# Optimization experiments

Measured on AMD Instinct MI355X. Metric: run time of the kernel, lower is better.

Reference implementation:

```python
import jax, jax.numpy as jnp
import numpy as np

N, H, W, PD, HID, NH = 2, 64, 64, 16, 128, 4
EPS = 1e-5


def _bn(x, g, b):
    # training-mode BatchNorm over (N, H, W) with biased variance, channels last
    m = jnp.mean(x, axis=(0, 1, 2), keepdims=True)
    v = jnp.var(x, axis=(0, 1, 2), keepdims=True)
    return (x - m) * jax.lax.rsqrt(v + EPS) * g + b


def _mha(x, in_w, in_b, out_w, out_b, nh):
    # torch nn.MultiheadAttention (batch_first) with packed qkv in_proj
    B, S, E = x.shape
    hd = E // nh
    q, k, v = jnp.split(x @ in_w.T + in_b, 3, axis=-1)
    def heads(t):
        return t.reshape(B, S, nh, hd).transpose(0, 2, 1, 3)  # B,nh,S,hd
    q, k, v = heads(q), heads(k), heads(v)
    a = jax.nn.softmax(jnp.einsum('bnqd,bnkd->bnqk', q, k) / np.float32(np.sqrt(hd)), axis=-1)
    o = jnp.einsum('bnqk,bnkd->bnqd', a, v).transpose(0, 2, 1, 3).reshape(B, S, E)
    return o @ out_w.T + out_b


def setup_inputs():
    key = jax.random.key(0)
    ks = jax.random.split(key, 32)
    def r(i, shape, s=0.1):
        return jax.random.normal(ks[i], shape, dtype=jnp.float32) * s
    mask = (jnp.arange(W) % 2) == 0  # alternating columns kept, M = W//2
    return {
        'kspace': jax.random.normal(ks[0], (N, 2, H, W), dtype=jnp.float32),
        'mask': mask,
        'pre_conv_w': r(1, (PD, 2), 0.5), 'pre_conv_b': r(2, (PD,)),
        'pre_pe_H': r(3, (H, PD)), 'pre_pe_W': r(4, (W, PD)),
        'res_conv1_w': r(5, (PD, PD), 0.2), 'res_conv1_b': r(6, (PD,)),
        'res_bn1_g': 1.0 + r(7, (PD,)), 'res_bn1_b': r(8, (PD,)),
        'res_conv2_w': r(9, (PD, PD), 0.2), 'res_conv2_b': r(10, (PD,)),
        'res_bn2_g': 1.0 + r(11, (PD,)), 'res_bn2_b': r(12, (PD,)),
        'proj_w': r(13, (HID, PD), 0.2), 'proj_b': r(14, (HID,)),
        'enc_in_w': r(15, (3 * HID, HID), 0.08), 'enc_in_b': r(16, (3 * HID,)),
        'enc_out_w': r(17, (HID, HID), 0.08), 'enc_out_b': r(18, (HID,)),
        'dec_pe_H': r(19, (H, HID)), 'dec_pe_W': r(20, (W, HID)),
        'dec_in_w': r(21, (3 * HID, HID), 0.08), 'dec_in_b': r(22, (3 * HID,)),
        'dec_out_w': r(23, (HID, HID), 0.08), 'dec_out_b': r(24, (HID,)),
        'masked_token': r(25, (HID,), 1.0),
        'post_w': r(26, (2, HID), 0.1), 'post_b': r(27, (2,)),
    }


def reference(kspace, mask, pre_conv_w, pre_conv_b, pre_pe_H, pre_pe_W,
              res_conv1_w, res_conv1_b, res_bn1_g, res_bn1_b,
              res_conv2_w, res_conv2_b, res_bn2_g, res_bn2_b,
              proj_w, proj_b, enc_in_w, enc_in_b, enc_out_w, enc_out_b,
              dec_pe_H, dec_pe_W, dec_in_w, dec_in_b, dec_out_w, dec_out_b,
              masked_token, post_w, post_b):
    cols = np.nonzero(np.asarray(mask))[0]  # static sampled columns
    M = cols.shape[0]
    # gather valid columns; channels last: [N, H, M, 2]
    x = kspace.transpose(0, 2, 3, 1)[:, :, cols, :]
    h = x @ pre_conv_w.T + pre_conv_b  # 1x1 conv -> [N, H, M, PD]
    h = h + (pre_pe_H[:, None, :] + pre_pe_W[cols][None, :, :])
    # PixelwiseConstantChannelResNet (1 layer)
    r1 = jax.nn.relu(_bn(h @ res_conv1_w.T + res_conv1_b, res_bn1_g, res_bn1_b))
    r2 = jax.nn.relu(_bn(r1 @ res_conv2_w.T + res_conv2_b, res_bn2_g, res_bn2_b))
    h = jax.nn.relu(h + r2)
    h = h @ proj_w.T + proj_b  # [N, H, M, HID]
    enc = _mha(h.reshape(N, H * M, HID), enc_in_w, enc_in_b, enc_out_w, enc_out_b, NH)
    # scatter: fill unmasked positions with masked_token, masked with encoder output
    dec = jnp.broadcast_to(masked_token, (N, H, W, HID))
    dec = dec.at[:, :, cols, :].set(enc.reshape(N, H, M, HID))
    dec = dec + (dec_pe_H[:, None, :] + dec_pe_W[None, :, :])
    dec = _mha(dec.reshape(N, H * W, HID), dec_in_w, dec_in_b, dec_out_w, dec_out_b, NH)
    out = dec.reshape(N, H, W, HID) @ post_w.T + post_b  # [N, H, W, 2]
    return out.transpose(0, 3, 1, 2)  # [N, 2, H, W]
```

## Files before the change

### kernel.cpp

```cpp
#include <hip/hip_runtime.h>
#include <math.h>

#define N_ 2
#define H_ 64
#define W_ 64
#define M_ 32
#define PD_ 16
#define HID_ 128
#define NH_ 4
#define HD_ 32
#define S_ENC 2048
#define S_DEC 4096
#define EPS_ 1e-5f
#define SCALE_ 0.17677669529663687f
#define SCALE2_ (0.17677669529663687f * 1.4426950408889634f)

#define OFF_H     0
#define OFF_T1    65536
#define OFF_T2    131072
#define OFF_STAT  196608
#define OFF_WP    196672
#define OFF_BP    202816
#define OFF_QBF   203264
#define OFF_KBF   727552
#define OFF_VTBF  1251840
#define OFF_ATTBF 1776128
#define OFF_XBF2  2300416
#define OFF_WBF   2824704

#define WOFF_ENC_OUT 0
#define WOFF_DEC_IN  16384
#define WOFF_DEC_OUT 65536

#define IB_MF   2048
#define IB_WC   320
#define IB_WP   24
#define IB_BP   2
#define IB_TOT  (IB_MF + IB_WC + IB_WP + IB_BP + 1)

typedef short bf16x8 __attribute__((ext_vector_type(8)));
typedef short bf16x4 __attribute__((ext_vector_type(4)));
typedef float f32x4 __attribute__((ext_vector_type(4)));

__device__ __forceinline__ short f2bf(float f) {
  union { float f; unsigned u; } v; v.f = f;
  unsigned r = v.u + 0x7FFFu + ((v.u >> 16) & 1u);
  return (short)(r >> 16);
}

__global__ void k_init(const float* __restrict__ eow, const float* __restrict__ dw,
                       const float* __restrict__ dow, const float* __restrict__ mt,
                       const float* __restrict__ peH, const float* __restrict__ peW,
                       const float* __restrict__ ew, const float* __restrict__ pw,
                       const float* __restrict__ pb, const float* __restrict__ eib,
                       short* __restrict__ wbf, short* __restrict__ xdec,
                       float* __restrict__ wp, float* __restrict__ bp,
                       float* __restrict__ stat) {
  int blk = blockIdx.x, tid = threadIdx.x;
  if (blk < IB_MF) {
    int idx = blk * 256 + tid;
    int j = idx & 127;
    int widx = (idx >> 7) & 31;
    int hh = (idx >> 12) & 63;
    int b = idx >> 18;
    int w = 2 * widx + 1;
    xdec[((size_t)(b * 4096 + hh * 64 + w)) * 128 + j] =
        f2bf(mt[j] + peH[hh * 128 + j] + peW[w * 128 + j]);
  } else if (blk < IB_MF + IB_WC) {
    int idx = (blk - IB_MF) * 256 + tid;
    float v;
    if (idx < 16384) v = eow[idx];
    else if (idx < 65536) v = dw[idx - 16384];
    else v = dow[idx - 65536];
    wbf[idx] = f2bf(v);
  } else if (blk < IB_MF + IB_WC + IB_WP) {
    int e = (blk - IB_MF - IB_WC) * 256 + tid;
    int row = e >> 4, k = e & 15;
    float a = 0.f;
    for (int j = 0; j < 128; j++) a = fmaf(ew[row * 128 + j], pw[j * 16 + k], a);
    wp[e] = a;
  } else if (blk < IB_MF + IB_WC + IB_WP + IB_BP) {
    int row = (blk - IB_MF - IB_WC - IB_WP) * 256 + tid;
    if (row < 384) {
      float a = eib[row];
      for (int j = 0; j < 128; j++) a = fmaf(ew[row * 128 + j], pb[j], a);
      bp[row] = a;
    }
  } else {
    if (tid < 64) stat[tid] = 0.f;
  }
}

__global__ void k_prelin_stats(const float* __restrict__ ks, const float* __restrict__ pcw,
                               const float* __restrict__ pcb, const float* __restrict__ peH,
                               const float* __restrict__ peW, const float* __restrict__ w1,
                               const float* __restrict__ b1, float* __restrict__ h,
                               float* __restrict__ t1, float* __restrict__ stat) {
  int tid = threadIdx.x;
  int pos = blockIdx.x * 256 + tid;
  int m = pos & 31, hh = (pos >> 5) & 63, b = pos >> 11;
  int w = 2 * m;
  float x0 = ks[((b * 2 + 0) * H_ + hh) * W_ + w];
  float x1 = ks[((b * 2 + 1) * H_ + hh) * W_ + w];
  float hv[16], tv[16];
#pragma unroll
  for (int c = 0; c < 16; c++)
    hv[c] = x0 * pcw[c * 2] + x1 * pcw[c * 2 + 1] + pcb[c]
            + peH[hh * PD_ + c] + peW[w * PD_ + c];
#pragma unroll
  for (int c = 0; c < 16; c += 4)
    *(float4*)&h[pos * 16 + c] = make_float4(hv[c], hv[c + 1], hv[c + 2], hv[c + 3]);
#pragma unroll
  for (int c = 0; c < 16; c++) {
    float a = b1[c];
#pragma unroll
    for (int k = 0; k < 16; k++) a = fmaf(hv[k], w1[c * 16 + k], a);
    tv[c] = a;
    t1[pos * 16 + c] = a;
  }
  __shared__ float tl[256][17];
#pragma unroll
  for (int c = 0; c < 16; c++) tl[tid][c] = tv[c];
  __syncthreads();
  int c = tid & 15, g = tid >> 4;
  float s = 0.f, s2 = 0.f;
#pragma unroll
  for (int r = 0; r < 16; r++) {
    float v = tl[g * 16 + r][c];
    s += v; s2 += v * v;
  }
  __shared__ float ps[16][16], ps2[16][16];
  ps[g][c] = s; ps2[g][c] = s2;
  __syncthreads();
  if (tid < 16) {
    float S = 0.f, S2 = 0.f;
#pragma unroll
    for (int g2 = 0; g2 < 16; g2++) { S += ps[g2][tid]; S2 += ps2[g2][tid]; }
    atomicAdd(&stat[tid], S);
    atomicAdd(&stat[16 + tid], S2);
  }
}

__global__ void k_bnlin_stats(const float* __restrict__ t1, const float* __restrict__ stat,
                              const float* __restrict__ g1, const float* __restrict__ bb1,
                              const float* __restrict__ w2, const float* __restrict__ b2,
                              float* __restrict__ t2, float* __restrict__ statw) {
  int tid = threadIdx.x;
  int pos = blockIdx.x * 256 + tid;
  const float inv = 1.f / 4096.f;
  float r[16];
#pragma unroll
  for (int k = 0; k < 16; k++) {
    float mu = stat[k] * inv;
    float var = stat[16 + k] * inv - mu * mu;
    float v = (t1[pos * 16 + k] - mu) * rsqrtf(var + EPS_) * g1[k] + bb1[k];
    r[k] = fmaxf(v, 0.f);
  }
  float tv[16];
#pragma unroll
  for (int c = 0; c < 16; c++) {
    float a = b2[c];
#pragma unroll
    for (int k = 0; k < 16; k++) a = fmaf(r[k], w2[c * 16 + k], a);
    tv[c] = a;
    t2[pos * 16 + c] = a;
  }
  __shared__ float tl[256][17];
#pragma unroll
  for (int c = 0; c < 16; c++) tl[tid][c] = tv[c];
  __syncthreads();
  int c = tid & 15, g = tid >> 4;
  float s = 0.f, s2 = 0.f;
#pragma unroll
  for (int rr = 0; rr < 16; rr++) {
    float v = tl[g * 16 + rr][c];
    s += v; s2 += v * v;
  }
  __shared__ float ps[16][16], ps2[16][16];
  ps[g][c] = s; ps2[g][c] = s2;
  __syncthreads();
  if (tid < 16) {
    float S = 0.f, S2 = 0.f;
#pragma unroll
    for (int g2 = 0; g2 < 16; g2++) { S += ps[g2][tid]; S2 += ps2[g2][tid]; }
    atomicAdd(&statw[32 + tid], S);
    atomicAdd(&statw[48 + tid], S2);
  }
}

__global__ __launch_bounds__(256)
void k_fqkv_enc(const float* __restrict__ h, const float* __restrict__ t2,
                const float* __restrict__ stat, const float* __restrict__ g2,
                const float* __restrict__ bb2, const float* __restrict__ wp,
                const float* __restrict__ bp, short* __restrict__ qbf,
                short* __restrict__ kbf, short* __restrict__ vtbf) {
  int tid = threadIdx.x;
  int p0 = blockIdx.x * 32;
  __shared__ float hf[32][20];
  const float inv = 1.f / 4096.f;
#pragma unroll
  for (int i = 0; i < 2; i++) {
    int idx = tid * 2 + i;
    int lp = idx >> 4, c = idx & 15;
    int pos = p0 + lp;
    float mu = stat[32 + c] * inv;
    float var = stat[48 + c] * inv - mu * mu;
    float v = (t2[pos * 16 + c] - mu) * rsqrtf(var + EPS_) * g2[c] + bb2[c];
    v = fmaxf(v, 0.f);
    hf[lp][c] = fmaxf(h[pos * 16 + c] + v, 0.f);
  }
  __syncthreads();
  int bb = p0 >> 11;
  int sbase = p0 & 2047;
  {
    int col = tid;
    float wc[16];
#pragma unroll
    for (int k = 0; k < 16; k += 4) *(float4*)&wc[k] = *(const float4*)&wp[col * 16 + k];
    float bpv = bp[col];
    int isQ = (col < 128);
    int c2 = isQ ? col : (col - 128);
    int hd = c2 >> 5, d = c2 & 31;
    short* dst = isQ ? qbf : kbf;
    float sc = isQ ? SCALE2_ : 1.f;
    size_t rowb = ((size_t)(bb * 4 + hd) * S_ENC + sbase) * 32 + d;
    for (int lp = 0; lp < 32; lp++) {
      float a = bpv;
#pragma unroll
      for (int k = 0; k < 16; k++) a = fmaf(hf[lp][k], wc[k], a);
      dst[rowb + (size_t)lp * 32] = f2bf(a * sc);
    }
  }
  if (tid < 128) {
    int col = 256 + tid;
    float wc[16];
#pragma unroll
    for (int k = 0; k < 16; k += 4) *(float4*)&wc[k] = *(const float4*)&wp[col * 16 + k];
    float bpv = bp[col];
    int c2 = tid;
    int hd = c2 >> 5, d = c2 & 31;
    size_t rowb = ((size_t)(bb * 4 + hd) * 32 + d) * S_ENC + sbase;
    for (int lp4 = 0; lp4 < 32; lp4 += 4) {
      bf16x4 pk;
#pragma unroll
      for (int r = 0; r < 4; r++) {
        float a = bpv;
#pragma unroll
        for (int k = 0; k < 16; k++) a = fmaf(hf[lp4 + r][k], wc[k], a);
        pk[r] = f2bf(a);
      }
      *(bf16x4*)&vtbf[rowb + lp4] = pk;
    }
  }
}

#define MGEMM_STAGE_AND_FRAGS                                                   \
  __shared__ short As[64 * 128];                                                \
  __shared__ short Wl[64 * 128];                                                \
  int tid = threadIdx.x;                                                        \
  _Pragma("unroll")                                                             \
  for (int i = 0; i < 4; i++) {                                                 \
    int idx = i * 256 + tid;                                                    \
    int row = idx >> 4, c = idx & 15, slot = c ^ (row & 7);                     \
    *(bf16x8*)&As[row * 128 + slot * 8] =                                       \
        *(const bf16x8*)&abf[(size_t)(rb + row) * 128 + c * 8];                 \
    *(bf16x8*)&Wl[row * 128 + slot * 8] =                                       \
        *(const bf16x8*)&wbf[(size_t)(ob + row) * 128 + c * 8];                 \
  }                                                                             \
  __syncthreads();                                                              \
  int lane = tid & 63, wv = tid >> 6;                                           \
  int l15 = lane & 15, quad = lane >> 4;                                        \
  int m0 = wv * 16;                                                             \
  f32x4 acc[4];                                                                 \
  acc[0] = acc[1] = acc[2] = acc[3] = (f32x4){0.f, 0.f, 0.f, 0.f};              \
  _Pragma("unroll")                                                             \
  for (int kk = 0; kk < 4; kk++) {                                              \
    int sl = ((kk * 4 + quad) ^ (l15 & 7)) * 8;                                 \
    bf16x8 af = *(const bf16x8*)&As[(m0 + l15) * 128 + sl];                     \
    _Pragma("unroll")                                                           \
    for (int nt = 0; nt < 4; nt++) {                                            \
      bf16x8 wf = *(const bf16x8*)&Wl[(nt * 16 + l15) * 128 + sl];              \
      acc[nt] = __builtin_amdgcn_mfma_f32_16x16x32_bf16(af, wf, acc[nt], 0, 0, 0); \
    }                                                                           \
  }

__global__ __launch_bounds__(256)
void k_mgemm_qkv_dec(const short* __restrict__ abf, const short* __restrict__ wbf,
                     const float* __restrict__ bias, short* __restrict__ qbf,
                     short* __restrict__ kbf, short* __restrict__ vtbf) {
  const int S = 4096;
  int rb = blockIdx.x * 64, ob = blockIdx.y * 64;
  MGEMM_STAGE_AND_FRAGS
#pragma unroll
  for (int nt = 0; nt < 4; nt++) {
    int col = ob + nt * 16 + l15;
    float bv = bias[col];
    if (ob < 128) {
      int hd = col >> 5, d = col & 31;
#pragma unroll
      for (int r = 0; r < 4; r++) {
        int grow = rb + m0 + quad * 4 + r;
        int bb = grow >> 12, s = grow & (S - 1);
        qbf[((size_t)(bb * 4 + hd) * S + s) * 32 + d] =
            f2bf((acc[nt][r] + bv) * SCALE2_);
      }
    } else if (ob < 256) {
      int c2 = col - 128, hd = c2 >> 5, d = c2 & 31;
#pragma unroll
      for (int r = 0; r < 4; r++) {
        int grow = rb + m0 + quad * 4 + r;
        int bb = grow >> 12, s = grow & (S - 1);
        kbf[((size_t)(bb * 4 + hd) * S + s) * 32 + d] = f2bf(acc[nt][r] + bv);
      }
    } else {
      int c2 = col - 256, hd = c2 >> 5, d = c2 & 31;
      int grow0 = rb + m0 + quad * 4;
      int bb = grow0 >> 12, s0 = grow0 & (S - 1);
      bf16x4 pk;
#pragma unroll
      for (int r = 0; r < 4; r++) pk[r] = f2bf(acc[nt][r] + bv);
      *(bf16x4*)&vtbf[((size_t)(bb * 4 + hd) * 32 + d) * S + s0] = pk;
    }
  }
}

__global__ __launch_bounds__(256)
void k_mgemm_out_enc(const short* __restrict__ abf, const short* __restrict__ wbf,
                     const float* __restrict__ bias, const float* __restrict__ peH,
                     const float* __restrict__ peW, short* __restrict__ xdec) {
  int rb = blockIdx.x * 64, ob = blockIdx.y * 64;
  MGEMM_STAGE_AND_FRAGS
#pragma unroll
  for (int nt = 0; nt < 4; nt++) {
    int col = ob + nt * 16 + l15;
    float bv = bias[col];
#pragma unroll
    for (int r = 0; r < 4; r++) {
      int grow = rb + m0 + quad * 4 + r;
      int bb = grow >> 11, rem = grow & 2047;
      int hhh = rem >> 5, m = rem & 31, w = 2 * m;
      xdec[((size_t)(bb * 4096 + hhh * 64 + w)) * 128 + col] =
          f2bf(acc[nt][r] + bv + peH[hhh * 128 + col] + peW[w * 128 + col]);
    }
  }
}

__global__ __launch_bounds__(256)
void k_mgemm_out_post(const short* __restrict__ abf, const short* __restrict__ wbf,
                      const float* __restrict__ bias, const float* __restrict__ pw,
                      const float* __restrict__ pb, float* __restrict__ outp) {
  int rb = blockIdx.x * 64;
  __shared__ short As[64 * 128];
  __shared__ short Wl[128 * 128];
  int tid = threadIdx.x;
#pragma unroll
  for (int i = 0; i < 4; i++) {
    int idx = i * 256 + tid;
    int row = idx >> 4, c = idx & 15, slot = c ^ (row & 7);
    *(bf16x8*)&As[row * 128 + slot * 8] =
        *(const bf16x8*)&abf[(size_t)(rb + row) * 128 + c * 8];
  }
#pragma unroll
  for (int i = 0; i < 8; i++) {
    int idx = i * 256 + tid;
    int row = idx >> 4, c = idx & 15, slot = c ^ (row & 7);
    *(bf16x8*)&Wl[row * 128 + slot * 8] =
        *(const bf16x8*)&wbf[(size_t)row * 128 + c * 8];
  }
  __syncthreads();
  int lane = tid & 63, wv = tid >> 6;
  int l15 = lane & 15, quad = lane >> 4;
  int m0 = wv * 16;
  f32x4 acc[8];
#pragma unroll
  for (int nt = 0; nt < 8; nt++) acc[nt] = (f32x4){0.f, 0.f, 0.f, 0.f};
#pragma unroll
  for (int kk = 0; kk < 4; kk++) {
    int sl = ((kk * 4 + quad) ^ (l15 & 7)) * 8;
    bf16x8 af = *(const bf16x8*)&As[(m0 + l15) * 128 + sl];
#pragma unroll
    for (int nt = 0; nt < 8; nt++) {
      bf16x8 wf = *(const bf16x8*)&Wl[(nt * 16 + l15) * 128 + sl];
      acc[nt] = __builtin_amdgcn_mfma_f32_16x16x32_bf16(af, wf, acc[nt], 0, 0, 0);
    }
  }
  float bv[8], pw0[8], pw1[8];
#pragma unroll
  for (int nt = 0; nt < 8; nt++) {
    int col = nt * 16 + l15;
    bv[nt] = bias[col];
    pw0[nt] = pw[col];
    pw1[nt] = pw[128 + col];
  }
  float pb0 = pb[0], pb1 = pb[1];
#pragma unroll
  for (int r = 0; r < 4; r++) {
    float pc0 = 0.f, pc1 = 0.f;
#pragma unroll
    for (int nt = 0; nt < 8; nt++) {
      float yv = acc[nt][r] + bv[nt];
      pc0 = fmaf(yv, pw0[nt], pc0);
      pc1 = fmaf(yv, pw1[nt], pc1);
    }
    pc0 += __shfl_xor(pc0, 1); pc0 += __shfl_xor(pc0, 2);
    pc0 += __shfl_xor(pc0, 4); pc0 += __shfl_xor(pc0, 8);
    pc1 += __shfl_xor(pc1, 1); pc1 += __shfl_xor(pc1, 2);
    pc1 += __shfl_xor(pc1, 4); pc1 += __shfl_xor(pc1, 8);
    if (l15 == 0) {
      int grow = rb + m0 + quad * 4 + r;
      int bb = grow >> 12, hw = grow & 4095;
      outp[(size_t)(bb * 2 + 0) * 4096 + hw] = pc0 + pb0;
      outp[(size_t)(bb * 2 + 1) * 4096 + hw] = pc1 + pb1;
    }
  }
}

template <int S>
__global__ __launch_bounds__(1024)
__attribute__((amdgpu_waves_per_eu(8)))
void k_attn15(const short* __restrict__ qbf, const short* __restrict__ kbf,
              const short* __restrict__ vtbf, short* __restrict__ outb) {
  __shared__ __align__(16) char smem[65536];
  short* kb4 = (short*)smem;
  short* vt4 = (short*)(smem + 32768);
  float* abuf = (float*)smem;
  float* lb   = (float*)(smem + 24576);

  int qt = blockIdx.x, hh = blockIdx.y, b = blockIdx.z;
  int tid = threadIdx.x;
  int lane = tid & 63;
  int wv = tid >> 6;
  int qtr = wv >> 2;
  int wv4 = wv & 3;
  int l15 = lane & 15, quad = lane >> 4;
  int t256 = tid & 255;

  int bh = b * NH_ + hh;
  const short* kg = kbf + (size_t)bh * S * 32;
  const short* vg = vtbf + (size_t)bh * 32 * S;
  short* kbh = kb4 + qtr * 2048;
  short* vth = vt4 + qtr * 2048;

  bf16x8 qf = *(const bf16x8*)&qbf[((size_t)bh * S + qt * 64 + wv4 * 16 + l15) * 32
                                   + quad * 8];

  f32x4 acc[2];
  acc[0] = (f32x4){0.f, 0.f, 0.f, 0.f};
  acc[1] = (f32x4){0.f, 0.f, 0.f, 0.f};
  f32x4 accl = (f32x4){0.f, 0.f, 0.f, 0.f};
  const short ONEB = (short)0x3F80;
  const bf16x8 ones = {ONEB, ONEB, ONEB, ONEB, ONEB, ONEB, ONEB, ONEB};

  int srowK = t256 >> 2, schK = t256 & 3;
  int slotK = schK ^ ((srowK >> 1) & 3);
  int srowV = t256 >> 3, sslV = t256 & 7;
  int sgV = sslV ^ (srowV & 7);
  int gbV = ((sgV >> 2) << 5) + ((sgV & 3) << 2);

  int kq0 = qtr * (S / 4);
  int kxor = (l15 >> 1) & 3;
  int vsl = l15 & 7;

  const short* kgp = kg + (size_t)(kq0 + srowK) * 32 + schK * 8;
  const short* vgp0 = vg + (size_t)srowV * S + kq0 + gbV;
  const short* vgp1 = vgp0 + 16;
  short* kdst = kbh + srowK * 32 + slotK * 8;
  short* vdst = vth + srowV * 64 + sslV * 8;

  bf16x8 krg = *(const bf16x8*)kgp;
  bf16x4 vr0 = *(const bf16x4*)vgp0;
  bf16x4 vr1 = *(const bf16x4*)vgp1;

  constexpr int NIT = S / 256;
  for (int it = 0; it < NIT; ++it) {
    int co = (it & 1) << 13;
    *(bf16x8*)(kdst + co) = krg;
    *(bf16x8*)(vdst + co) = __builtin_shufflevector(vr0, vr1, 0, 1, 2, 3, 4, 5, 6, 7);
    if (it + 1 < NIT) {
      kgp += 64 * 32;
      vgp0 += 64;
      vgp1 += 64;
      krg = *(const bf16x8*)kgp;
      vr0 = *(const bf16x4*)vgp0;
      vr1 = *(const bf16x4*)vgp1;
    }
    asm volatile("s_waitcnt lgkmcnt(0)" ::: "memory");
    __builtin_amdgcn_s_barrier();
    asm volatile("" ::: "memory");

    const short* kbhc = kbh + co;
    const short* vthc = vth + co;

    f32x4 s[4];
#pragma unroll
    for (int t = 0; t < 4; t++) {
      bf16x8 kf = *(const bf16x8*)&kbhc[(t * 16 + l15) * 32 + ((quad ^ kxor) * 8)];
      s[t] = __builtin_amdgcn_mfma_f32_16x16x32_bf16(
          kf, qf, (f32x4){0.f, 0.f, 0.f, 0.f}, 0, 0, 0);
    }

    float pe[4][4];
#pragma unroll
    for (int t = 0; t < 4; t++) {
      pe[t][0] = __builtin_exp2f(s[t][0]);
      pe[t][1] = __builtin_exp2f(s[t][1]);
      pe[t][2] = __builtin_exp2f(s[t][2]);
      pe[t][3] = __builtin_exp2f(s[t][3]);
    }

#pragma unroll
    for (int kh = 0; kh < 2; kh++) {
      union { unsigned u[4]; bf16x8 v; } pf;
      asm("v_cvt_pk_bf16_f32 %0, %1, %2"
          : "=v"(pf.u[0]) : "v"(pe[2 * kh][0]), "v"(pe[2 * kh][1]));
      asm("v_cvt_pk_bf16_f32 %0, %1, %2"
          : "=v"(pf.u[1]) : "v"(pe[2 * kh][2]), "v"(pe[2 * kh][3]));
      asm("v_cvt_pk_bf16_f32 %0, %1, %2"
          : "=v"(pf.u[2]) : "v"(pe[2 * kh + 1][0]), "v"(pe[2 * kh + 1][1]));
      asm("v_cvt_pk_bf16_f32 %0, %1, %2"
          : "=v"(pf.u[3]) : "v"(pe[2 * kh + 1][2]), "v"(pe[2 * kh + 1][3]));
#pragma unroll
      for (int nt = 0; nt < 2; nt++) {
        bf16x8 vf = *(const bf16x8*)&vthc[(nt * 16 + l15) * 64
                                          + (((kh * 4 + quad) ^ vsl) * 8)];
        acc[nt] = __builtin_amdgcn_mfma_f32_16x16x32_bf16(vf, pf.v, acc[nt], 0, 0, 0);
      }
      accl = __builtin_amdgcn_mfma_f32_16x16x32_bf16(ones, pf.v, accl, 0, 0, 0);
    }
  }

  float lpart = accl[0];

  __syncthreads();
  if (qtr > 0) {
#pragma unroll
    for (int nt = 0; nt < 2; nt++)
#pragma unroll
      for (int r = 0; r < 4; r++)
        abuf[(qtr - 1) * 2048 + wv4 * 512 + (nt * 16 + quad * 4 + r) * 16 + l15] =
            acc[nt][r];
    if (quad == 0) lb[(qtr - 1) * 64 + wv4 * 16 + l15] = lpart;
  }
  __syncthreads();
  if (qtr == 0) {
    int li = wv4 * 16 + l15;
    float ltot = lpart + lb[li] + lb[64 + li] + lb[128 + li];
    float inv = 1.f / ltot;
    int base = wv4 * 512;
    short* op = outb + ((size_t)(b * S + qt * 64 + wv4 * 16 + l15)) * 128 + hh * 32;
#pragma unroll
    for (int nt = 0; nt < 2; nt++) {
      bf16x4 pk;
#pragma unroll
      for (int r = 0; r < 4; r++) {
        int d = nt * 16 + quad * 4 + r;
        float v = acc[nt][r] + abuf[base + d * 16 + l15]
                + abuf[2048 + base + d * 16 + l15]
                + abuf[4096 + base + d * 16 + l15];
        pk[r] = f2bf(v * inv);
      }
      *(bf16x4*)&op[nt * 16 + quad * 4] = pk;
    }
  }
}

template <int S>
__global__ __launch_bounds__(1024, 4)
void k_attn16(const short* __restrict__ qbf, const short* __restrict__ kbf,
              const short* __restrict__ vtbf, short* __restrict__ outb) {
  __shared__ __align__(16) char smem[65536];
  short* kb4 = (short*)smem;
  short* vt4 = (short*)(smem + 32768);
  float* abuf = (float*)smem;
  float* lb   = (float*)(smem + 49152);

  int qt = blockIdx.x, hh = blockIdx.y, b = blockIdx.z;
  int tid = threadIdx.x;
  int lane = tid & 63;
  int wv = tid >> 6;
  int qtr = wv >> 2;
  int qsub = wv & 3;
  int l15 = lane & 15, quad = lane >> 4;
  int t256 = tid & 255;

  int bh = b * NH_ + hh;
  const short* kg = kbf + (size_t)bh * S * 32;
  const short* vg = vtbf + (size_t)bh * 32 * S;
  short* kbh = kb4 + qtr * 2048;
  short* vth = vt4 + qtr * 2048;

  const short* qrow = &qbf[((size_t)bh * S + qt * 128 + qsub * 32 + l15) * 32
                           + quad * 8];
  bf16x8 qf0 = *(const bf16x8*)qrow;
  bf16x8 qf1 = *(const bf16x8*)(qrow + 16 * 32);

  f32x4 acc00 = {0.f,0.f,0.f,0.f}, acc01 = {0.f,0.f,0.f,0.f};
  f32x4 acc10 = {0.f,0.f,0.f,0.f}, acc11 = {0.f,0.f,0.f,0.f};
  f32x4 accl0 = {0.f,0.f,0.f,0.f}, accl1 = {0.f,0.f,0.f,0.f};
  const short ONEB = (short)0x3F80;
  const bf16x8 ones = {ONEB, ONEB, ONEB, ONEB, ONEB, ONEB, ONEB, ONEB};

  int srowK = t256 >> 2, schK = t256 & 3;
  int slotK = schK ^ ((srowK >> 1) & 3);
  int srowV = t256 >> 3, sslV = t256 & 7;
  int sgV = sslV ^ (srowV & 7);
  int gbV = ((sgV >> 2) << 5) + ((sgV & 3) << 2);

  int kq0 = qtr * (S / 4);
  int kxor = (l15 >> 1) & 3;
  int vsl = l15 & 7;

  const short* kgp = kg + (size_t)(kq0 + srowK) * 32 + schK * 8;
  const short* vgp0 = vg + (size_t)srowV * S + kq0 + gbV;
  const short* vgp1 = vgp0 + 16;
  short* kdst = kbh + srowK * 32 + slotK * 8;
  short* vdst = vth + srowV * 64 + sslV * 8;

  bf16x8 krg = *(const bf16x8*)kgp;
  bf16x4 vr0 = *(const bf16x4*)vgp0;
  bf16x4 vr1 = *(const bf16x4*)vgp1;

  constexpr int NIT = S / 256;
  for (int it = 0; it < NIT; ++it) {
    int co = (it & 1) << 13;
    *(bf16x8*)(kdst + co) = krg;
    *(bf16x8*)(vdst + co) = __builtin_shufflevector(vr0, vr1, 0, 1, 2, 3, 4, 5, 6, 7);
    if (it + 1 < NIT) {
      kgp += 64 * 32;
      vgp0 += 64;
      vgp1 += 64;
      krg = *(const bf16x8*)kgp;
      vr0 = *(const bf16x4*)vgp0;
      vr1 = *(const bf16x4*)vgp1;
    }
    asm volatile("s_waitcnt lgkmcnt(0)" ::: "memory");
    __builtin_amdgcn_s_barrier();
    asm volatile("" ::: "memory");

    const short* kbhc = kbh + co;
    const short* vthc = vth + co;

    f32x4 s0[4], s1[4];
#pragma unroll
    for (int t = 0; t < 4; t++) {
      bf16x8 kf = *(const bf16x8*)&kbhc[(t * 16 + l15) * 32 + ((quad ^ kxor) * 8)];
      s0[t] = __builtin_amdgcn_mfma_f32_16x16x32_bf16(
          kf, qf0, (f32x4){0.f, 0.f, 0.f, 0.f}, 0, 0, 0);
      s1[t] = __builtin_amdgcn_mfma_f32_16x16x32_bf16(
          kf, qf1, (f32x4){0.f, 0.f, 0.f, 0.f}, 0, 0, 0);
    }

#pragma unroll
    for (int kh = 0; kh < 2; kh++) {
      bf16x8 vfa = *(const bf16x8*)&vthc[(0 * 16 + l15) * 64
                                         + (((kh * 4 + quad) ^ vsl) * 8)];
      bf16x8 vfb = *(const bf16x8*)&vthc[(1 * 16 + l15) * 64
                                         + (((kh * 4 + quad) ^ vsl) * 8)];
      {
        float pa0 = __builtin_exp2f(s0[2 * kh][0]);
        float pa1 = __builtin_exp2f(s0[2 * kh][1]);
        float pa2 = __builtin_exp2f(s0[2 * kh][2]);
        float pa3 = __builtin_exp2f(s0[2 * kh][3]);
        float pb0v = __builtin_exp2f(s0[2 * kh + 1][0]);
        float pb1v = __builtin_exp2f(s0[2 * kh + 1][1]);
        float pb2v = __builtin_exp2f(s0[2 * kh + 1][2]);
        float pb3v = __builtin_exp2f(s0[2 * kh + 1][3]);
        union { unsigned u[4]; bf16x8 v; } pf;
        asm("v_cvt_pk_bf16_f32 %0, %1, %2" : "=v"(pf.u[0]) : "v"(pa0), "v"(pa1));
        asm("v_cvt_pk_bf16_f32 %0, %1, %2" : "=v"(pf.u[1]) : "v"(pa2), "v"(pa3));
        asm("v_cvt_pk_bf16_f32 %0, %1, %2" : "=v"(pf.u[2]) : "v"(pb0v), "v"(pb1v));
        asm("v_cvt_pk_bf16_f32 %0, %1, %2" : "=v"(pf.u[3]) : "v"(pb2v), "v"(pb3v));
        acc00 = __builtin_amdgcn_mfma_f32_16x16x32_bf16(vfa, pf.v, acc00, 0, 0, 0);
        acc01 = __builtin_amdgcn_mfma_f32_16x16x32_bf16(vfb, pf.v, acc01, 0, 0, 0);
        accl0 = __builtin_amdgcn_mfma_f32_16x16x32_bf16(ones, pf.v, accl0, 0, 0, 0);
      }
      {
        float pa0 = __builtin_exp2f(s1[2 * kh][0]);
        float pa1 = __builtin_exp2f(s1[2 * kh][1]);
        float pa2 = __builtin_exp2f(s1[2 * kh][2]);
        float pa3 = __builtin_exp2f(s1[2 * kh][3]);
        float pb0v = __builtin_exp2f(s1[2 * kh + 1][0]);
        float pb1v = __builtin_exp2f(s1[2 * kh + 1][1]);
        float pb2v = __builtin_exp2f(s1[2 * kh + 1][2]);
        float pb3v = __builtin_exp2f(s1[2 * kh + 1][3]);
        union { unsigned u[4]; bf16x8 v; } pf;
        asm("v_cvt_pk_bf16_f32 %0, %1, %2" : "=v"(pf.u[0]) : "v"(pa0), "v"(pa1));
        asm("v_cvt_pk_bf16_f32 %0, %1, %2" : "=v"(pf.u[1]) : "v"(pa2), "v"(pa3));
        asm("v_cvt_pk_bf16_f32 %0, %1, %2" : "=v"(pf.u[2]) : "v"(pb0v), "v"(pb1v));
        asm("v_cvt_pk_bf16_f32 %0, %1, %2" : "=v"(pf.u[3]) : "v"(pb2v), "v"(pb3v));
        acc10 = __builtin_amdgcn_mfma_f32_16x16x32_bf16(vfa, pf.v, acc10, 0, 0, 0);
        acc11 = __builtin_amdgcn_mfma_f32_16x16x32_bf16(vfb, pf.v, acc11, 0, 0, 0);
        accl1 = __builtin_amdgcn_mfma_f32_16x16x32_bf16(ones, pf.v, accl1, 0, 0, 0);
      }
    }
  }

  __syncthreads();
  if (qtr > 0) {
    float* ab = abuf + (qtr - 1) * 4096 + (qsub * 2) * 512;
#pragma unroll
    for (int r = 0; r < 4; r++) {
      ab[(0 * 16 + quad * 4 + r) * 16 + l15] = acc00[r];
      ab[(1 * 16 + quad * 4 + r) * 16 + l15] = acc01[r];
      ab[512 + (0 * 16 + quad * 4 + r) * 16 + l15] = acc10[r];
      ab[512 + (1 * 16 + quad * 4 + r) * 16 + l15] = acc11[r];
    }
    if (quad == 0) {
      lb[(qtr - 1) * 128 + qsub * 32 + l15] = accl0[0];
      lb[(qtr - 1) * 128 + qsub * 32 + 16 + l15] = accl1[0];
    }
  }
  __syncthreads();
  if (qtr == 0) {
#pragma unroll
    for (int j = 0; j < 2; j++) {
      int li = qsub * 32 + j * 16 + l15;
      float lpart = (j == 0) ? accl0[0] : accl1[0];
      float ltot = lpart + lb[li] + lb[128 + li] + lb[256 + li];
      float inv = 1.f / ltot;
      int base = (qsub * 2 + j) * 512;
      f32x4 a0 = (j == 0) ? acc00 : acc10;
      f32x4 a1 = (j == 0) ? acc01 : acc11;
      short* op = outb + ((size_t)(b * S + qt * 128 + li)) * 128 + hh * 32;
#pragma unroll
      for (int nt = 0; nt < 2; nt++) {
        bf16x4 pk;
#pragma unroll
        for (int r = 0; r < 4; r++) {
          int d = nt * 16 + quad * 4 + r;
          float v = ((nt == 0) ? a0[r] : a1[r])
                  + abuf[base + d * 16 + l15]
                  + abuf[4096 + base + d * 16 + l15]
                  + abuf[8192 + base + d * 16 + l15];
          pk[r] = f2bf(v * inv);
        }
        *(bf16x4*)&op[nt * 16 + quad * 4] = pk;
      }
    }
  }
}

extern "C" void kernel_launch(void* const* d_in, const int* in_sizes, int n_in,
                              void* d_out, int out_size, void* d_ws, size_t ws_size,
                              hipStream_t stream) {
  const float* ks        = (const float*)d_in[0];
  const float* pre_conv_w = (const float*)d_in[2];
  const float* pre_conv_b = (const float*)d_in[3];
  const float* pre_pe_H   = (const float*)d_in[4];
  const float* pre_pe_W   = (const float*)d_in[5];
  const float* w1  = (const float*)d_in[6];
  const float* b1  = (const float*)d_in[7];
  const float* g1  = (const float*)d_in[8];
  const float* bb1 = (const float*)d_in[9];
  const float* w2  = (const float*)d_in[10];
  const float* b2  = (const float*)d_in[11];
  const float* g2  = (const float*)d_in[12];
  const float* bb2 = (const float*)d_in[13];
  const float* proj_w = (const float*)d_in[14];
  const float* proj_b = (const float*)d_in[15];
  const float* enc_in_w  = (const float*)d_in[16];
  const float* enc_in_b  = (const float*)d_in[17];
  const float* enc_out_w = (const float*)d_in[18];
  const float* enc_out_b = (const float*)d_in[19];
  const float* dec_pe_H  = (const float*)d_in[20];
  const float* dec_pe_W  = (const float*)d_in[21];
  const float* dec_in_w  = (const float*)d_in[22];
  const float* dec_in_b  = (const float*)d_in[23];
  const float* dec_out_w = (const float*)d_in[24];
  const float* dec_out_b = (const float*)d_in[25];
  const float* masked_token = (const float*)d_in[26];
  const float* post_w = (const float*)d_in[27];
  const float* post_b = (const float*)d_in[28];
  float* out = (float*)d_out;

  float* ws    = (float*)d_ws;
  float* h     = ws + OFF_H;
  float* t1    = ws + OFF_T1;
  float* t2    = ws + OFF_T2;
  float* stat  = ws + OFF_STAT;
  float* wp    = ws + OFF_WP;
  float* bp    = ws + OFF_BP;
  short* qbf   = (short*)(ws + OFF_QBF);
  short* kbfb  = (short*)(ws + OFF_KBF);
  short* vtbfb = (short*)(ws + OFF_VTBF);
  short* attbf = (short*)(ws + OFF_ATTBF);
  short* xbf2  = (short*)(ws + OFF_XBF2);
  short* wbf   = (short*)(ws + OFF_WBF);

  k_init<<<IB_TOT, 256, 0, stream>>>(enc_out_w, dec_in_w, dec_out_w, masked_token,
                                     dec_pe_H, dec_pe_W, enc_in_w, proj_w, proj_b,
                                     enc_in_b, wbf, xbf2, wp, bp, stat);
  k_prelin_stats<<<16, 256, 0, stream>>>(ks, pre_conv_w, pre_conv_b, pre_pe_H,
                                         pre_pe_W, w1, b1, h, t1, stat);
  k_bnlin_stats<<<16, 256, 0, stream>>>(t1, stat, g1, bb1, w2, b2, t2, stat);
  k_fqkv_enc<<<128, 256, 0, stream>>>(h, t2, stat, g2, bb2, wp, bp,
                                      qbf, kbfb, vtbfb);
  k_attn15<S_ENC><<<dim3(S_ENC / 64, NH_, N_), 1024, 0, stream>>>(qbf, kbfb, vtbfb, attbf);
  k_mgemm_out_enc<<<dim3(S_ENC * N_ / 64, 2), 256, 0, stream>>>(
      attbf, wbf + WOFF_ENC_OUT, enc_out_b, dec_pe_H, dec_pe_W, xbf2);
  k_mgemm_qkv_dec<<<dim3(S_DEC * N_ / 64, 6), 256, 0, stream>>>(
      xbf2, wbf + WOFF_DEC_IN, dec_in_b, qbf, kbfb, vtbfb);
  k_attn16<S_DEC><<<dim3(S_DEC / 128, NH_, N_), 1024, 0, stream>>>(qbf, kbfb, vtbfb, attbf);
  k_mgemm_out_post<<<S_DEC * N_ / 64, 256, 0, stream>>>(
      attbf, wbf + WOFF_DEC_OUT, dec_out_b, post_w, post_b, out);
}
```

Baseline: 196.1 us.

## Split decoder attention keys across blocks and merge partials in out-projection

The decoder attention kernel no longer uses 1024-thread blocks that split the keys four ways and reduce through shared memory. It now launches 256-thread blocks that each handle half of the keys for one head. Each block writes its unnormalized bf16 partial output and float row-sum to workspace. The output-projection GEMM then adds the two halves and applies the normalization while loading its A tile. This removes the in-block LDS reduction and barriers and allows more, smaller blocks, at the cost of extra global traffic for the partials and an extra bf16 rounding step before the combine.

```diff
diff --git a/kernel.cpp b/kernel.cpp
--- a/kernel.cpp
+++ b/kernel.cpp
@@ -46,6 +46,12 @@
   union { float f; unsigned u; } v; v.f = f;
   unsigned r = v.u + 0x7FFFu + ((v.u >> 16) & 1u);
   return (short)(r >> 16);
+}
+
+__device__ __forceinline__ float bf2f(short s) {
+  union { unsigned u; float f; } v;
+  v.u = ((unsigned)(unsigned short)s) << 16;
+  return v.f;
 }
 
 __global__ void k_init(const float* __restrict__ eow, const float* __restrict__ dw,
@@ -346,9 +352,12 @@
 }
 
 __global__ __launch_bounds__(256)
-void k_mgemm_out_post(const short* __restrict__ abf, const short* __restrict__ wbf,
+void k_mgemm_out_post(const short* __restrict__ pbf, const float* __restrict__ lp,
+                      const short* __restrict__ wbf,
                       const float* __restrict__ bias, const float* __restrict__ pw,
                       const float* __restrict__ pb, float* __restrict__ outp) {
+  const int S = 4096;
+  const size_t HSTRIDE = (size_t)N_ * S * 128;
   int rb = blockIdx.x * 64;
   __shared__ short As[64 * 128];
   __shared__ short Wl[128 * 128];
@@ -357,8 +366,18 @@
   for (int i = 0; i < 4; i++) {
     int idx = i * 256 + tid;
     int row = idx >> 4, c = idx & 15, slot = c ^ (row & 7);
-    *(bf16x8*)&As[row * 128 + slot * 8] =
-        *(const bf16x8*)&abf[(size_t)(rb + row) * 128 + c * 8];
+    int grow = rb + row;
+    int bb = grow >> 12, q = grow & (S - 1);
+    int hh = c >> 2;
+    size_t lidx = (size_t)(bb * 4 + hh) * S + q;
+    float lt = lp[lidx] + lp[(size_t)8 * S + lidx];
+    float inv = 1.f / lt;
+    bf16x8 p0 = *(const bf16x8*)&pbf[(size_t)grow * 128 + c * 8];
+    bf16x8 p1 = *(const bf16x8*)&pbf[HSTRIDE + (size_t)grow * 128 + c * 8];
+    bf16x8 o;
+#pragma unroll
+    for (int j = 0; j < 8; j++) o[j] = f2bf((bf2f(p0[j]) + bf2f(p1[j])) * inv);
+    *(bf16x8*)&As[row * 128 + slot * 8] = o;
   }
 #pragma unroll
   for (int i = 0; i < 8; i++) {
@@ -565,29 +584,21 @@
 }
 
 template <int S>
-__global__ __launch_bounds__(1024, 4)
-void k_attn16(const short* __restrict__ qbf, const short* __restrict__ kbf,
-              const short* __restrict__ vtbf, short* __restrict__ outb) {
-  __shared__ __align__(16) char smem[65536];
-  short* kb4 = (short*)smem;
-  short* vt4 = (short*)(smem + 32768);
-  float* abuf = (float*)smem;
-  float* lb   = (float*)(smem + 49152);
-
-  int qt = blockIdx.x, hh = blockIdx.y, b = blockIdx.z;
+__global__ __launch_bounds__(256, 2)
+void k_attn18(const short* __restrict__ qbf, const short* __restrict__ kbf,
+              const short* __restrict__ vtbf, short* __restrict__ op,
+              float* __restrict__ lp) {
+  __shared__ __align__(16) short kb[4096];
+  __shared__ __align__(16) short vt[4096];
+
+  int qt = blockIdx.x, half = blockIdx.y, bh = blockIdx.z;
   int tid = threadIdx.x;
   int lane = tid & 63;
-  int wv = tid >> 6;
-  int qtr = wv >> 2;
-  int qsub = wv & 3;
+  int qsub = tid >> 6;
   int l15 = lane & 15, quad = lane >> 4;
-  int t256 = tid & 255;
-
-  int bh = b * NH_ + hh;
+
   const short* kg = kbf + (size_t)bh * S * 32;
   const short* vg = vtbf + (size_t)bh * 32 * S;
-  short* kbh = kb4 + qtr * 2048;
-  short* vth = vt4 + qtr * 2048;
 
   const short* qrow = &qbf[((size_t)bh * S + qt * 128 + qsub * 32 + l15) * 32
                            + quad * 8];
@@ -600,29 +611,29 @@
   const short ONEB = (short)0x3F80;
   const bf16x8 ones = {ONEB, ONEB, ONEB, ONEB, ONEB, ONEB, ONEB, ONEB};
 
-  int srowK = t256 >> 2, schK = t256 & 3;
+  int srowK = tid >> 2, schK = tid & 3;
   int slotK = schK ^ ((srowK >> 1) & 3);
-  int srowV = t256 >> 3, sslV = t256 & 7;
+  int srowV = tid >> 3, sslV = tid & 7;
   int sgV = sslV ^ (srowV & 7);
   int gbV = ((sgV >> 2) << 5) + ((sgV & 3) << 2);
 
-  int kq0 = qtr * (S / 4);
+  int kq0 = half * (S / 2);
   int kxor = (l15 >> 1) & 3;
   int vsl = l15 & 7;
 
   const short* kgp = kg + (size_t)(kq0 + srowK) * 32 + schK * 8;
   const short* vgp0 = vg + (size_t)srowV * S + kq0 + gbV;
   const short* vgp1 = vgp0 + 16;
-  short* kdst = kbh + srowK * 32 + slotK * 8;
-  short* vdst = vth + srowV * 64 + sslV * 8;
+  short* kdst = kb + srowK * 32 + slotK * 8;
+  short* vdst = vt + srowV * 64 + sslV * 8;
 
   bf16x8 krg = *(const bf16x8*)kgp;
   bf16x4 vr0 = *(const bf16x4*)vgp0;
   bf16x4 vr1 = *(const bf16x4*)vgp1;
 
-  constexpr int NIT = S / 256;
+  constexpr int NIT = S / 128;
   for (int it = 0; it < NIT; ++it) {
-    int co = (it & 1) << 13;
+    int co = (it & 1) << 11;
     *(bf16x8*)(kdst + co) = krg;
     *(bf16x8*)(vdst + co) = __builtin_shufflevector(vr0, vr1, 0, 1, 2, 3, 4, 5, 6, 7);
     if (it + 1 < NIT) {
@@ -637,8 +648,8 @@
     __builtin_amdgcn_s_barrier();
     asm volatile("" ::: "memory");
 
-    const short* kbhc = kbh + co;
-    const short* vthc = vth + co;
+    const short* kbhc = kb + co;
+    const short* vthc = vt + co;
 
     f32x4 s0[4], s1[4];
 #pragma unroll
@@ -695,48 +706,23 @@
     }
   }
 
-  __syncthreads();
-  if (qtr > 0) {
-    float* ab = abuf + (qtr - 1) * 4096 + (qsub * 2) * 512;
-#pragma unroll
-    for (int r = 0; r < 4; r++) {
-      ab[(0 * 16 + quad * 4 + r) * 16 + l15] = acc00[r];
-      ab[(1 * 16 + quad * 4 + r) * 16 + l15] = acc01[r];
-      ab[512 + (0 * 16 + quad * 4 + r) * 16 + l15] = acc10[r];
-      ab[512 + (1 * 16 + quad * 4 + r) * 16 + l15] = acc11[r];
-    }
-    if (quad == 0) {
-      lb[(qtr - 1) * 128 + qsub * 32 + l15] = accl0[0];
-      lb[(qtr - 1) * 128 + qsub * 32 + 16 + l15] = accl1[0];
-    }
-  }
-  __syncthreads();
-  if (qtr == 0) {
-#pragma unroll
-    for (int j = 0; j < 2; j++) {
-      int li = qsub * 32 + j * 16 + l15;
-      float lpart = (j == 0) ? accl0[0] : accl1[0];
-      float ltot = lpart + lb[li] + lb[128 + li] + lb[256 + li];
-      float inv = 1.f / ltot;
-      int base = (qsub * 2 + j) * 512;
-      f32x4 a0 = (j == 0) ? acc00 : acc10;
-      f32x4 a1 = (j == 0) ? acc01 : acc11;
-      short* op = outb + ((size_t)(b * S + qt * 128 + li)) * 128 + hh * 32;
-#pragma unroll
-      for (int nt = 0; nt < 2; nt++) {
-        bf16x4 pk;
-#pragma unroll
-        for (int r = 0; r < 4; r++) {
-          int d = nt * 16 + quad * 4 + r;
-          float v = ((nt == 0) ? a0[r] : a1[r])
-                  + abuf[base + d * 16 + l15]
-                  + abuf[4096 + base + d * 16 + l15]
-                  + abuf[8192 + base + d * 16 + l15];
-          pk[r] = f2bf(v * inv);
-        }
-        *(bf16x4*)&op[nt * 16 + quad * 4] = pk;
-      }
-    }
+  int b = bh >> 2, hhd = bh & 3;
+  short* ob = op + (size_t)half * ((size_t)N_ * S * 128)
+            + ((size_t)(b * S + qt * 128 + qsub * 32)) * 128 + hhd * 32;
+  bf16x4 w00, w01, w10, w11;
+#pragma unroll
+  for (int r = 0; r < 4; r++) {
+    w00[r] = f2bf(acc00[r]); w01[r] = f2bf(acc01[r]);
+    w10[r] = f2bf(acc10[r]); w11[r] = f2bf(acc11[r]);
+  }
+  *(bf16x4*)&ob[(size_t)(0 * 16 + l15) * 128 + 0 * 16 + quad * 4] = w00;
+  *(bf16x4*)&ob[(size_t)(0 * 16 + l15) * 128 + 1 * 16 + quad * 4] = w01;
+  *(bf16x4*)&ob[(size_t)(1 * 16 + l15) * 128 + 0 * 16 + quad * 4] = w10;
+  *(bf16x4*)&ob[(size_t)(1 * 16 + l15) * 128 + 1 * 16 + quad * 4] = w11;
+  if (quad == 0) {
+    float* lb = lp + (size_t)(half * 8 + bh) * S + qt * 128 + qsub * 32;
+    lb[l15] = accl0[0];
+    lb[16 + l15] = accl1[0];
   }
 }
 
@@ -800,7 +786,8 @@
       attbf, wbf + WOFF_ENC_OUT, enc_out_b, dec_pe_H, dec_pe_W, xbf2);
   k_mgemm_qkv_dec<<<dim3(S_DEC * N_ / 64, 6), 256, 0, stream>>>(
       xbf2, wbf + WOFF_DEC_IN, dec_in_b, qbf, kbfb, vtbfb);
-  k_attn16<S_DEC><<<dim3(S_DEC / 128, NH_, N_), 1024, 0, stream>>>(qbf, kbfb, vtbfb, attbf);
+  k_attn18<S_DEC><<<dim3(S_DEC / 128, 2, NH_ * N_), 256, 0, stream>>>(
+      qbf, kbfb, vtbfb, attbf, h);
   k_mgemm_out_post<<<S_DEC * N_ / 64, 256, 0, stream>>>(
-      attbf, wbf + WOFF_DEC_OUT, dec_out_b, post_w, post_b, out);
-}
+      attbf, h, wbf + WOFF_DEC_OUT, dec_out_b, post_w, post_b, out);
+}
```

Result: slower. 205.9 us (+5.0%).

## Split decoder attention keys across two blocks and merge partials in out-proj GEMM

Applied to the files above, without the earlier changes.

The decoder attention kernel now splits the key range into two halves across a new grid dimension, doubling block count. Each block writes unnormalized bf16 partial outputs plus row sums to workspace. The output-projection GEMM adds the two partials and normalizes during its A-tile staging. This gives more parallelism on a 128-block grid, at the cost of extra global traffic and bf16 rounding of unnormalized partials. The merge assumes both halves share the same max; this holds only because the kernel does not subtract a running max.

```diff
diff --git a/kernel.cpp b/kernel.cpp
--- a/kernel.cpp
+++ b/kernel.cpp
@@ -46,6 +46,12 @@
   union { float f; unsigned u; } v; v.f = f;
   unsigned r = v.u + 0x7FFFu + ((v.u >> 16) & 1u);
   return (short)(r >> 16);
+}
+
+__device__ __forceinline__ float bf2f(short s) {
+  union { unsigned u; float f; } v;
+  v.u = ((unsigned)(unsigned short)s) << 16;
+  return v.f;
 }
 
 __global__ void k_init(const float* __restrict__ eow, const float* __restrict__ dw,
@@ -346,9 +352,12 @@
 }
 
 __global__ __launch_bounds__(256)
-void k_mgemm_out_post(const short* __restrict__ abf, const short* __restrict__ wbf,
+void k_mgemm_out_post(const short* __restrict__ pbf, const float* __restrict__ lp,
+                      const short* __restrict__ wbf,
                       const float* __restrict__ bias, const float* __restrict__ pw,
                       const float* __restrict__ pb, float* __restrict__ outp) {
+  const int S = 4096;
+  const size_t HSTRIDE = (size_t)N_ * S * 128;
   int rb = blockIdx.x * 64;
   __shared__ short As[64 * 128];
   __shared__ short Wl[128 * 128];
@@ -357,8 +366,18 @@
   for (int i = 0; i < 4; i++) {
     int idx = i * 256 + tid;
     int row = idx >> 4, c = idx & 15, slot = c ^ (row & 7);
-    *(bf16x8*)&As[row * 128 + slot * 8] =
-        *(const bf16x8*)&abf[(size_t)(rb + row) * 128 + c * 8];
+    int grow = rb + row;
+    int bb = grow >> 12, q = grow & (S - 1);
+    int hh = c >> 2;
+    size_t lidx = (size_t)(bb * 4 + hh) * S + q;
+    float lt = lp[lidx] + lp[(size_t)8 * S + lidx];
+    float inv = 1.f / lt;
+    bf16x8 p0 = *(const bf16x8*)&pbf[(size_t)grow * 128 + c * 8];
+    bf16x8 p1 = *(const bf16x8*)&pbf[HSTRIDE + (size_t)grow * 128 + c * 8];
+    bf16x8 o;
+#pragma unroll
+    for (int j = 0; j < 8; j++) o[j] = f2bf((bf2f(p0[j]) + bf2f(p1[j])) * inv);
+    *(bf16x8*)&As[row * 128 + slot * 8] = o;
   }
 #pragma unroll
   for (int i = 0; i < 8; i++) {
@@ -565,16 +584,17 @@
 }
 
 template <int S>
-__global__ __launch_bounds__(1024, 4)
-void k_attn16(const short* __restrict__ qbf, const short* __restrict__ kbf,
-              const short* __restrict__ vtbf, short* __restrict__ outb) {
+__global__ __launch_bounds__(1024, 8)
+void k_attn19(const short* __restrict__ qbf, const short* __restrict__ kbf,
+              const short* __restrict__ vtbf, short* __restrict__ op,
+              float* __restrict__ lp) {
   __shared__ __align__(16) char smem[65536];
   short* kb4 = (short*)smem;
   short* vt4 = (short*)(smem + 32768);
   float* abuf = (float*)smem;
   float* lb   = (float*)(smem + 49152);
 
-  int qt = blockIdx.x, hh = blockIdx.y, b = blockIdx.z;
+  int qt = blockIdx.x, half = blockIdx.y, bh = blockIdx.z;
   int tid = threadIdx.x;
   int lane = tid & 63;
   int wv = tid >> 6;
@@ -583,7 +603,6 @@
   int l15 = lane & 15, quad = lane >> 4;
   int t256 = tid & 255;
 
-  int bh = b * NH_ + hh;
   const short* kg = kbf + (size_t)bh * S * 32;
   const short* vg = vtbf + (size_t)bh * 32 * S;
   short* kbh = kb4 + qtr * 2048;
@@ -606,7 +625,7 @@
   int sgV = sslV ^ (srowV & 7);
   int gbV = ((sgV >> 2) << 5) + ((sgV & 3) << 2);
 
-  int kq0 = qtr * (S / 4);
+  int kq0 = half * (S / 2) + qtr * (S / 8);
   int kxor = (l15 >> 1) & 3;
   int vsl = l15 & 7;
 
@@ -620,7 +639,7 @@
   bf16x4 vr0 = *(const bf16x4*)vgp0;
   bf16x4 vr1 = *(const bf16x4*)vgp1;
 
-  constexpr int NIT = S / 256;
+  constexpr int NIT = S / 512;
   for (int it = 0; it < NIT; ++it) {
     int co = (it & 1) << 13;
     *(bf16x8*)(kdst + co) = krg;
@@ -695,6 +714,8 @@
     }
   }
 
+  float lpart0 = accl0[0], lpart1 = accl1[0];
+
   __syncthreads();
   if (qtr > 0) {
     float* ab = abuf + (qtr - 1) * 4096 + (qsub * 2) * 512;
@@ -706,22 +727,24 @@
       ab[512 + (1 * 16 + quad * 4 + r) * 16 + l15] = acc11[r];
     }
     if (quad == 0) {
-      lb[(qtr - 1) * 128 + qsub * 32 + l15] = accl0[0];
-      lb[(qtr - 1) * 128 + qsub * 32 + 16 + l15] = accl1[0];
+      lb[(qtr - 1) * 128 + qsub * 32 + l15] = lpart0;
+      lb[(qtr - 1) * 128 + qsub * 32 + 16 + l15] = lpart1;
     }
   }
   __syncthreads();
   if (qtr == 0) {
+    const size_t HSTRIDE = (size_t)N_ * S * 128;
+    int b = bh >> 2, hhd = bh & 3;
 #pragma unroll
     for (int j = 0; j < 2; j++) {
       int li = qsub * 32 + j * 16 + l15;
-      float lpart = (j == 0) ? accl0[0] : accl1[0];
+      float lpart = (j == 0) ? lpart0 : lpart1;
       float ltot = lpart + lb[li] + lb[128 + li] + lb[256 + li];
-      float inv = 1.f / ltot;
       int base = (qsub * 2 + j) * 512;
       f32x4 a0 = (j == 0) ? acc00 : acc10;
       f32x4 a1 = (j == 0) ? acc01 : acc11;
-      short* op = outb + ((size_t)(b * S + qt * 128 + li)) * 128 + hh * 32;
+      short* opp = op + (size_t)half * HSTRIDE
+                 + ((size_t)(b * S + qt * 128 + li)) * 128 + hhd * 32;
 #pragma unroll
       for (int nt = 0; nt < 2; nt++) {
         bf16x4 pk;
@@ -732,10 +755,12 @@
                   + abuf[base + d * 16 + l15]
                   + abuf[4096 + base + d * 16 + l15]
                   + abuf[8192 + base + d * 16 + l15];
-          pk[r] = f2bf(v * inv);
+          pk[r] = f2bf(v);
         }
-        *(bf16x4*)&op[nt * 16 + quad * 4] = pk;
+        *(bf16x4*)&opp[nt * 16 + quad * 4] = pk;
       }
+      if (quad == 0)
+        lp[(size_t)(half * 8 + bh) * S + qt * 128 + li] = ltot;
     }
   }
 }
@@ -800,7 +825,8 @@
       attbf, wbf + WOFF_ENC_OUT, enc_out_b, dec_pe_H, dec_pe_W, xbf2);
   k_mgemm_qkv_dec<<<dim3(S_DEC * N_ / 64, 6), 256, 0, stream>>>(
       xbf2, wbf + WOFF_DEC_IN, dec_in_b, qbf, kbfb, vtbfb);
-  k_attn16<S_DEC><<<dim3(S_DEC / 128, NH_, N_), 1024, 0, stream>>>(qbf, kbfb, vtbfb, attbf);
+  k_attn19<S_DEC><<<dim3(S_DEC / 128, 2, NH_ * N_), 1024, 0, stream>>>(
+      qbf, kbfb, vtbfb, attbf, h);
   k_mgemm_out_post<<<S_DEC * N_ / 64, 256, 0, stream>>>(
-      attbf, wbf + WOFF_DEC_OUT, dec_out_b, post_w, post_b, out);
-}
+      attbf, h, wbf + WOFF_DEC_OUT, dec_out_b, post_w, post_b, out);
+}
```

New measurement: 296.7 us. 51.3% more time.
